# Performance work log

Hardware: AMD Instinct MI355X
Metric: run time of the kernel (lower is better)

The kernel has to match this reference:

```python
import jax, jax.numpy as jnp
import numpy as np

B, T, I, H, O, F = 256, 2048, 64, 256, 64, 16
NUM_LAYERS = 2


def setup_inputs() -> dict:
    key = jax.random.key(0)
    ks = jax.random.split(key, 12)
    s = 1.0 / np.sqrt(H)  # PyTorch RNN/Linear init scale
    u = lambda k, shp: jax.random.uniform(k, shp, jnp.float32, -s, s)
    return {
        "x": jax.random.normal(ks[0], (B, T, I), jnp.float32),
        "hidden": jnp.zeros((NUM_LAYERS, B, H), jnp.float32),
        "W_ih0": u(ks[1], (H, I)),
        "W_hh0": u(ks[2], (H, H)),
        "b_ih0": u(ks[3], (H,)),
        "b_hh0": u(ks[4], (H,)),
        "W_ih1": u(ks[5], (H, H)),
        "W_hh1": u(ks[6], (H, H)),
        "b_ih1": u(ks[7], (H,)),
        "b_hh1": u(ks[8], (H,)),
        "fc_W": u(ks[9], (O, H)),
        "fc_b": u(ks[10], (O,)),
        "future_timesegments": F,
    }


def _rnn_layer(xs, h0, W_ih, W_hh, b_ih, b_hh):
    # xs: [T, B, in_dim]; h0: [B, H]
    # Precompute input contribution for all timesteps (one big GEMM),
    # then scan only the sequential recurrence h@W_hh^T + tanh.
    pre = jnp.einsum('tbi,hi->tbh', xs, W_ih) + b_ih + b_hh  # [T, B, H]

    def step(h, p_t):
        h_new = jnp.tanh(p_t + h @ W_hh.T)
        return h_new, h_new

    h_T, ys = jax.lax.scan(step, h0, pre)
    return ys, h_T  # ys: [T, B, H]


def reference(x, hidden, W_ih0, W_hh0, b_ih0, b_hh0,
              W_ih1, W_hh1, b_ih1, b_hh1, fc_W, fc_b,
              future_timesegments):
    xs = jnp.swapaxes(x, 0, 1)  # [T, B, I] (batch_first -> time major)
    ys0, h0 = _rnn_layer(xs, hidden[0], W_ih0, W_hh0, b_ih0, b_hh0)
    ys1, h1 = _rnn_layer(ys0, hidden[1], W_ih1, W_hh1, b_ih1, b_hh1)
    # out[:, -F:, :] in batch-first layout
    tail = jnp.swapaxes(ys1[-future_timesegments:], 0, 1)  # [B, F, H]
    out = tail @ fc_W.T + fc_b  # [B, F, O]
    new_hidden = jnp.stack([h0, h1])  # [num_layers, B, H]
    return out, new_hidden
```

## Files before the change

### kernel.cpp

```cpp
#include <hip/hip_runtime.h>

#define BB 256
#define TT 2048
#define II 64
#define HH 256
#define OO 64
#define FF 16


#define BUFSZ 2048
#define BUF0 0
#define BUF1 BUFSZ
#define H1OFF 704
#define XOFF 1344
#define SLICE 80
#define TAILOFF (2 * BUFSZ)
#define LDSBYTES (TAILOFF + FF * HH * 2)

typedef _Float16 h2 __attribute__((ext_vector_type(2)));
typedef _Float16 h8 __attribute__((ext_vector_type(8)));

__device__ __forceinline__ float fdot2f(h2 a, h2 b, float c) {
#if __has_builtin(__builtin_amdgcn_fdot2)
  return __builtin_amdgcn_fdot2(a, b, c, false);
#else
  return c + (float)a[0] * (float)b[0] + (float)a[1] * (float)b[1];
#endif
}

__device__ __forceinline__ float fast_tanh(float z) {
  float e = __builtin_amdgcn_exp2f(z * 2.885390081777927f);
  return 1.0f - 2.0f * __builtin_amdgcn_rcpf(e + 1.0f);
}

__device__ __forceinline__ h2 i2h(int w) {
  union { int i; h2 h; } u; u.i = w; return u.h;
}
__device__ __forceinline__ int pk2i(const float* p) {
  union { h2 h; int i; } u; u.h[0] = (_Float16)p[0]; u.h[1] = (_Float16)p[1];
  return u.i;
}

template <int CTRL>
__device__ __forceinline__ float dpp_add(float v) {
  union { float f; int i; } a, r;
  a.f = v;
  r.i = __builtin_amdgcn_update_dpp(0, a.i, CTRL, 0xF, 0xF, true);
  return v + r.f;
}
__device__ __forceinline__ float swz4_add(float v) {
  union { float f; int i; } a, r;
  a.f = v;
  r.i = __builtin_amdgcn_ds_swizzle(a.i, 0x101F);
  return v + r.f;
}

#define RNN_STEP(T, RB, WB)                                                    \
  {                                                                            \
    float xn = 0.f;                                                            \
    if (kg == 0) {                                                             \
      int tn = (T) + 1 < TT ? (T) + 1 : (T);                                   \
      xn = xrow[(size_t)tn * II + xi];                                         \
    }                                                                          \
    float a0[4] = {0.f, 0.f, 0.f, 0.f};                                        \
    float a1[4] = {0.f, 0.f, 0.f, 0.f};                                        \
    {                                                                          \
      const int4 xv = *(const int4*)(xaddr + (RB) + XOFF);                     \
      _Pragma("unroll") for (int r = 0; r < 4; ++r) {                          \
        a0[r] = fdot2f(i2h(xv.x), i2h(w0x[r][0]), a0[r]);                      \
        a0[r] = fdot2f(i2h(xv.y), i2h(w0x[r][1]), a0[r]);                      \
        a0[r] = fdot2f(i2h(xv.z), i2h(w0x[r][2]), a0[r]);                      \
        a0[r] = fdot2f(i2h(xv.w), i2h(w0x[r][3]), a0[r]);                      \
      }                                                                        \
    }                                                                          \
    _Pragma("unroll") for (int c = 0; c < 4; ++c) {                            \
      const int4 v = *(const int4*)(haddr + (RB) + c * 16);                    \
      _Pragma("unroll") for (int r = 0; r < 4; ++r) {                          \
        a0[r] = fdot2f(i2h(v.x), i2h(w0h[r][4 * c + 0]), a0[r]);               \
        a0[r] = fdot2f(i2h(v.y), i2h(w0h[r][4 * c + 1]), a0[r]);               \
        a0[r] = fdot2f(i2h(v.z), i2h(w0h[r][4 * c + 2]), a0[r]);               \
        a0[r] = fdot2f(i2h(v.w), i2h(w0h[r][4 * c + 3]), a0[r]);               \
        a1[r] = fdot2f(i2h(v.x), i2h(w1g[r][4 * c + 0]), a1[r]);               \
        a1[r] = fdot2f(i2h(v.y), i2h(w1g[r][4 * c + 1]), a1[r]);               \
        a1[r] = fdot2f(i2h(v.z), i2h(w1g[r][4 * c + 2]), a1[r]);               \
        a1[r] = fdot2f(i2h(v.w), i2h(w1g[r][4 * c + 3]), a1[r]);               \
      }                                                                        \
    }                                                                          \
    _Pragma("unroll") for (int c = 0; c < 4; ++c) {                            \
      const int4 v = *(const int4*)(haddr + (RB) + H1OFF + c * 16);            \
      _Pragma("unroll") for (int r = 0; r < 4; ++r) {                          \
        a1[r] = fdot2f(i2h(v.x), i2h(w1h[r][4 * c + 0]), a1[r]);               \
        a1[r] = fdot2f(i2h(v.y), i2h(w1h[r][4 * c + 1]), a1[r]);               \
        a1[r] = fdot2f(i2h(v.z), i2h(w1h[r][4 * c + 2]), a1[r]);               \
        a1[r] = fdot2f(i2h(v.w), i2h(w1h[r][4 * c + 3]), a1[r]);               \
      }                                                                        \
    }                                                                          \
    _Pragma("unroll") for (int r = 0; r < 4; ++r) {                            \
      a0[r] = dpp_add<0xB1>(a0[r]);                                            \
      a0[r] = dpp_add<0x4E>(a0[r]);                                            \
      a0[r] = swz4_add(a0[r]);                                                 \
      a1[r] = dpp_add<0xB1>(a1[r]);                                            \
      a1[r] = dpp_add<0x4E>(a1[r]);                                            \
      a1[r] = swz4_add(a1[r]);                                                 \
    }                                                                          \
    float s0 = (kg & 1) ? a0[1] : a0[0];                                       \
    float s1 = (kg & 1) ? a0[3] : a0[2];                                       \
    float u0 = (kg & 1) ? a1[1] : a1[0];                                       \
    float u1 = (kg & 1) ? a1[3] : a1[2];                                       \
    float v0 = (kg & 2) ? s1 : s0;                                             \
    float v1 = (kg & 2) ? u1 : u0;                                             \
    float hnew = fast_tanh((L ? v1 : v0) + mybias);                            \
    hlast = hnew;                                                              \
    if ((T) > 0 || L == 0) *(_Float16*)(waddr + (WB)) = (_Float16)hnew;        \
    if (L == 1 && (T) >= TT - FF + 1)                                          \
      *(_Float16*)(tailaddr + ((T) - (TT - FF + 1)) * (HH * 2)) =              \
          (_Float16)hnew;                                                      \
    if (kg == 0) *(_Float16*)(lb + (WB) + XOFF + xi * 2) = (_Float16)xn;       \
    __syncthreads();                                                           \
  }

__global__ __attribute__((amdgpu_flat_work_group_size(512, 512),
                          amdgpu_waves_per_eu(2, 2)))
void rnn_fused(const float* __restrict__ x, const float* __restrict__ hidden,
               const float* __restrict__ Wih0, const float* __restrict__ Whh0,
               const float* __restrict__ bih0, const float* __restrict__ bhh0,
               const float* __restrict__ Wih1, const float* __restrict__ Whh1,
               const float* __restrict__ bih1, const float* __restrict__ bhh1,
               const float* __restrict__ fcW, const float* __restrict__ fcb,
               float* __restrict__ out)
{
  const int tid = threadIdx.x;
  const int b = blockIdx.x;
  const int lane = tid & 63;
  const int kg = lane & 7;
  const int rg = (tid >> 6) * 8 + (lane >> 3);
  const int j0 = rg * 4;
  const int L = kg >> 2;
  const int cj = j0 + (kg & 3);
  const int xi = tid >> 3;

  __shared__ __align__(16) char lds[LDSBYTES];
  char* lb = (char*)lds;

  int w0x[4][4], w0h[4][16], w1g[4][16], w1h[4][16];
#pragma unroll
  for (int r = 0; r < 4; ++r) {
    const float* p0 = Wih0 + (size_t)(j0 + r) * II + kg * 8;
#pragma unroll
    for (int m = 0; m < 4; ++m) w0x[r][m] = pk2i(p0 + 2 * m);
    const float* p1 = Whh0 + (size_t)(j0 + r) * HH + kg * 32;
#pragma unroll
    for (int m = 0; m < 16; ++m) w0h[r][m] = pk2i(p1 + 2 * m);
    const float* p2 = Wih1 + (size_t)(j0 + r) * HH + kg * 32;
#pragma unroll
    for (int m = 0; m < 16; ++m) w1g[r][m] = pk2i(p2 + 2 * m);
    const float* p3 = Whh1 + (size_t)(j0 + r) * HH + kg * 32;
#pragma unroll
    for (int m = 0; m < 16; ++m) w1h[r][m] = pk2i(p3 + 2 * m);
  }
#pragma unroll
  for (int r = 0; r < 4; ++r) {
#pragma unroll
    for (int m = 0; m < 4; ++m) asm volatile("" : "+v"(w0x[r][m]));
#pragma unroll
    for (int m = 0; m < 16; ++m) {
      asm volatile("" : "+v"(w0h[r][m]));
      asm volatile("" : "+v"(w1g[r][m]));
      asm volatile("" : "+v"(w1h[r][m]));
    }
  }
  float mybias = L ? (bih1[cj] + bhh1[cj]) : (bih0[cj] + bhh0[cj]);
  asm volatile("" : "+v"(mybias));

  const char* haddr = lb + kg * SLICE;
  const char* xaddr = lb + kg * 16;
  char* waddr = lb + L * H1OFF + (cj >> 5) * SLICE + (cj & 31) * 2;
  char* tailaddr = lb + TAILOFF + cj * 2;

  if (tid < HH) {
    char* p = lb + (tid >> 5) * SLICE + (tid & 31) * 2;
    _Float16 h0v = (_Float16)hidden[(size_t)b * HH + tid];
    _Float16 h1v = (_Float16)hidden[(size_t)(BB + b) * HH + tid];
    *(_Float16*)(p + BUF0) = h0v;
    *(_Float16*)(p + BUF0 + H1OFF) = h1v;
    *(_Float16*)(p + BUF1 + H1OFF) = h1v;
  }
  const float* xrow = x + (size_t)b * TT * II;
  if (tid < II) *(_Float16*)(lb + BUF0 + XOFF + tid * 2) = (_Float16)xrow[tid];
  float hlast = 0.f, h1last = 0.f;
  __syncthreads();

#pragma unroll 1
  for (int t = 0; t < TT; t += 2) {
    RNN_STEP(t, BUF0, BUF1)
    RNN_STEP(t + 1, BUF1, BUF0)
  }

  {
    float a1[4] = {0.f, 0.f, 0.f, 0.f};
#pragma unroll
    for (int c = 0; c < 4; ++c) {
      const int4 v = *(const int4*)(haddr + BUF0 + c * 16);
#pragma unroll
      for (int r = 0; r < 4; ++r) {
        a1[r] = fdot2f(i2h(v.x), i2h(w1g[r][4 * c + 0]), a1[r]);
        a1[r] = fdot2f(i2h(v.y), i2h(w1g[r][4 * c + 1]), a1[r]);
        a1[r] = fdot2f(i2h(v.z), i2h(w1g[r][4 * c + 2]), a1[r]);
        a1[r] = fdot2f(i2h(v.w), i2h(w1g[r][4 * c + 3]), a1[r]);
      }
    }
#pragma unroll
    for (int c = 0; c < 4; ++c) {
      const int4 v = *(const int4*)(haddr + BUF0 + H1OFF + c * 16);
#pragma unroll
      for (int r = 0; r < 4; ++r) {
        a1[r] = fdot2f(i2h(v.x), i2h(w1h[r][4 * c + 0]), a1[r]);
        a1[r] = fdot2f(i2h(v.y), i2h(w1h[r][4 * c + 1]), a1[r]);
        a1[r] = fdot2f(i2h(v.z), i2h(w1h[r][4 * c + 2]), a1[r]);
        a1[r] = fdot2f(i2h(v.w), i2h(w1h[r][4 * c + 3]), a1[r]);
      }
    }
#pragma unroll
    for (int r = 0; r < 4; ++r) {
      a1[r] = dpp_add<0xB1>(a1[r]);
      a1[r] = dpp_add<0x4E>(a1[r]);
      a1[r] = swz4_add(a1[r]);
    }
    float u0 = (kg & 1) ? a1[1] : a1[0];
    float u1 = (kg & 1) ? a1[3] : a1[2];
    float v1 = (kg & 2) ? u1 : u0;
    float h1e = fast_tanh(v1 + mybias);
    h1last = h1e;
    if (L == 1) *(_Float16*)(tailaddr + (FF - 1) * (HH * 2)) = (_Float16)h1e;
  }
  __syncthreads();

  if (L == 0) out[BB * FF * OO + (size_t)b * HH + cj] = hlast;
  else        out[BB * FF * OO + (size_t)(BB + b) * HH + cj] = h1last;

  const int o = tid & 63;
  const int fg = tid >> 6;
  const _Float16* tp = (const _Float16*)(lb + TAILOFF);
  float acc0 = 0.f, acc1 = 0.f;
  const float* wrow = fcW + o * HH;
  for (int c = 0; c < HH / 8; ++c) {
    float wv[8];
#pragma unroll
    for (int k = 0; k < 8; ++k) wv[k] = wrow[8 * c + k];
    h8 q0 = *(const h8*)(tp + (2 * fg) * HH + 8 * c);
    h8 q1 = *(const h8*)(tp + (2 * fg + 1) * HH + 8 * c);
#pragma unroll
    for (int e = 0; e < 8; ++e) {
      acc0 += (float)q0[e] * wv[e];
      acc1 += (float)q1[e] * wv[e];
    }
  }
  const float bo = fcb[o];
  out[((size_t)b * FF + 2 * fg) * OO + o] = acc0 + bo;
  out[((size_t)b * FF + 2 * fg + 1) * OO + o] = acc1 + bo;
}

extern "C" void kernel_launch(void* const* d_in, const int* in_sizes, int n_in,
                              void* d_out, int out_size, void* d_ws, size_t ws_size,
                              hipStream_t stream) {
  (void)in_sizes; (void)n_in; (void)d_ws; (void)ws_size; (void)out_size;
  rnn_fused<<<dim3(BB), dim3(512), 0, stream>>>(
      (const float*)d_in[0],  (const float*)d_in[1],
      (const float*)d_in[2],  (const float*)d_in[3],
      (const float*)d_in[4],  (const float*)d_in[5],
      (const float*)d_in[6],  (const float*)d_in[7],
      (const float*)d_in[8],  (const float*)d_in[9],
      (const float*)d_in[10], (const float*)d_in[11],
      (float*)d_out);
}
```

Baseline: 3.280 ms.

## Repartition RNN step to 4-way K split with 2 rows per thread

Changes the per-thread work split from an 8-way reduction split over 4 output rows to a 4-way split over 2 rows per thread, with longer K slices (64 elements). This removes the ds_swizzle reduction stage, leaving only two DPP adds, and cuts the select logic. The LDS layout of the hidden state and x is restrided to match. Dot products now go through inline-asm v_dot2_f32_f16. Weight registers per thread stay about the same, but each thread's serial dot-product chain doubles in length, which may lengthen the critical path of each sequential step.

```diff
diff --git a/kernel.cpp b/kernel.cpp
--- a/kernel.cpp
+++ b/kernel.cpp
@@ -8,24 +8,20 @@
 #define FF 16
 
 
-#define BUFSZ 2048
+#define BUFSZ 1280
 #define BUF0 0
 #define BUF1 BUFSZ
-#define H1OFF 704
-#define XOFF 1344
-#define SLICE 80
+#define H1OFF 576
+#define XOFF 1152
+#define HSL 144
+#define XSL 32
 #define TAILOFF (2 * BUFSZ)
 #define LDSBYTES (TAILOFF + FF * HH * 2)
 
-typedef _Float16 h2 __attribute__((ext_vector_type(2)));
 typedef _Float16 h8 __attribute__((ext_vector_type(8)));
 
-__device__ __forceinline__ float fdot2f(h2 a, h2 b, float c) {
-#if __has_builtin(__builtin_amdgcn_fdot2)
-  return __builtin_amdgcn_fdot2(a, b, c, false);
-#else
-  return c + (float)a[0] * (float)b[0] + (float)a[1] * (float)b[1];
-#endif
+__device__ __forceinline__ void adot(float& acc, int hv, int wv) {
+  asm("v_dot2_f32_f16 %0, %1, %2, %0" : "+v"(acc) : "v"(hv), "v"(wv));
 }
 
 __device__ __forceinline__ float fast_tanh(float z) {
@@ -33,11 +29,9 @@
   return 1.0f - 2.0f * __builtin_amdgcn_rcpf(e + 1.0f);
 }
 
-__device__ __forceinline__ h2 i2h(int w) {
-  union { int i; h2 h; } u; u.i = w; return u.h;
-}
 __device__ __forceinline__ int pk2i(const float* p) {
-  union { h2 h; int i; } u; u.h[0] = (_Float16)p[0]; u.h[1] = (_Float16)p[1];
+  union { _Float16 h[2]; int i; } u;
+  u.h[0] = (_Float16)p[0]; u.h[1] = (_Float16)p[1];
   return u.i;
 }
 
@@ -48,74 +42,55 @@
   r.i = __builtin_amdgcn_update_dpp(0, a.i, CTRL, 0xF, 0xF, true);
   return v + r.f;
 }
-__device__ __forceinline__ float swz4_add(float v) {
-  union { float f; int i; } a, r;
-  a.f = v;
-  r.i = __builtin_amdgcn_ds_swizzle(a.i, 0x101F);
-  return v + r.f;
-}
 
 #define RNN_STEP(T, RB, WB)                                                    \
   {                                                                            \
     float xn = 0.f;                                                            \
-    if (kg == 0) {                                                             \
+    if ((tid & 7) == 0) {                                                      \
       int tn = (T) + 1 < TT ? (T) + 1 : (T);                                   \
       xn = xrow[(size_t)tn * II + xi];                                         \
     }                                                                          \
-    float a0[4] = {0.f, 0.f, 0.f, 0.f};                                        \
-    float a1[4] = {0.f, 0.f, 0.f, 0.f};                                        \
-    {                                                                          \
-      const int4 xv = *(const int4*)(xaddr + (RB) + XOFF);                     \
-      _Pragma("unroll") for (int r = 0; r < 4; ++r) {                          \
-        a0[r] = fdot2f(i2h(xv.x), i2h(w0x[r][0]), a0[r]);                      \
-        a0[r] = fdot2f(i2h(xv.y), i2h(w0x[r][1]), a0[r]);                      \
-        a0[r] = fdot2f(i2h(xv.z), i2h(w0x[r][2]), a0[r]);                      \
-        a0[r] = fdot2f(i2h(xv.w), i2h(w0x[r][3]), a0[r]);                      \
-      }                                                                        \
-    }                                                                          \
-    _Pragma("unroll") for (int c = 0; c < 4; ++c) {                            \
-      const int4 v = *(const int4*)(haddr + (RB) + c * 16);                    \
-      _Pragma("unroll") for (int r = 0; r < 4; ++r) {                          \
-        a0[r] = fdot2f(i2h(v.x), i2h(w0h[r][4 * c + 0]), a0[r]);               \
-        a0[r] = fdot2f(i2h(v.y), i2h(w0h[r][4 * c + 1]), a0[r]);               \
-        a0[r] = fdot2f(i2h(v.z), i2h(w0h[r][4 * c + 2]), a0[r]);               \
-        a0[r] = fdot2f(i2h(v.w), i2h(w0h[r][4 * c + 3]), a0[r]);               \
-        a1[r] = fdot2f(i2h(v.x), i2h(w1g[r][4 * c + 0]), a1[r]);               \
-        a1[r] = fdot2f(i2h(v.y), i2h(w1g[r][4 * c + 1]), a1[r]);               \
-        a1[r] = fdot2f(i2h(v.z), i2h(w1g[r][4 * c + 2]), a1[r]);               \
-        a1[r] = fdot2f(i2h(v.w), i2h(w1g[r][4 * c + 3]), a1[r]);               \
-      }                                                                        \
-    }                                                                          \
-    _Pragma("unroll") for (int c = 0; c < 4; ++c) {                            \
-      const int4 v = *(const int4*)(haddr + (RB) + H1OFF + c * 16);            \
-      _Pragma("unroll") for (int r = 0; r < 4; ++r) {                          \
-        a1[r] = fdot2f(i2h(v.x), i2h(w1h[r][4 * c + 0]), a1[r]);               \
-        a1[r] = fdot2f(i2h(v.y), i2h(w1h[r][4 * c + 1]), a1[r]);               \
-        a1[r] = fdot2f(i2h(v.z), i2h(w1h[r][4 * c + 2]), a1[r]);               \
-        a1[r] = fdot2f(i2h(v.w), i2h(w1h[r][4 * c + 3]), a1[r]);               \
-      }                                                                        \
-    }                                                                          \
-    _Pragma("unroll") for (int r = 0; r < 4; ++r) {                            \
-      a0[r] = dpp_add<0xB1>(a0[r]);                                            \
-      a0[r] = dpp_add<0x4E>(a0[r]);                                            \
-      a0[r] = swz4_add(a0[r]);                                                 \
-      a1[r] = dpp_add<0xB1>(a1[r]);                                            \
-      a1[r] = dpp_add<0x4E>(a1[r]);                                            \
-      a1[r] = swz4_add(a1[r]);                                                 \
-    }                                                                          \
-    float s0 = (kg & 1) ? a0[1] : a0[0];                                       \
-    float s1 = (kg & 1) ? a0[3] : a0[2];                                       \
-    float u0 = (kg & 1) ? a1[1] : a1[0];                                       \
-    float u1 = (kg & 1) ? a1[3] : a1[2];                                       \
-    float v0 = (kg & 2) ? s1 : s0;                                             \
-    float v1 = (kg & 2) ? u1 : u0;                                             \
+    float a00 = 0.f, a01 = 0.f, a10 = 0.f, a11 = 0.f;                          \
+    _Pragma("unroll") for (int c = 0; c < 2; ++c) {                            \
+      const int4 v = *(const int4*)(xaddr + (RB) + c * 16);                    \
+      adot(a00, v.x, w0x[0][4 * c + 0]); adot(a00, v.y, w0x[0][4 * c + 1]);    \
+      adot(a00, v.z, w0x[0][4 * c + 2]); adot(a00, v.w, w0x[0][4 * c + 3]);    \
+      adot(a01, v.x, w0x[1][4 * c + 0]); adot(a01, v.y, w0x[1][4 * c + 1]);    \
+      adot(a01, v.z, w0x[1][4 * c + 2]); adot(a01, v.w, w0x[1][4 * c + 3]);    \
+    }                                                                          \
+    _Pragma("unroll") for (int c = 0; c < 8; ++c) {                            \
+      const int4 v = *(const int4*)(h0addr + (RB) + c * 16);                   \
+      adot(a00, v.x, w0h[0][4 * c + 0]); adot(a00, v.y, w0h[0][4 * c + 1]);    \
+      adot(a00, v.z, w0h[0][4 * c + 2]); adot(a00, v.w, w0h[0][4 * c + 3]);    \
+      adot(a01, v.x, w0h[1][4 * c + 0]); adot(a01, v.y, w0h[1][4 * c + 1]);    \
+      adot(a01, v.z, w0h[1][4 * c + 2]); adot(a01, v.w, w0h[1][4 * c + 3]);    \
+      adot(a10, v.x, w1g[0][4 * c + 0]); adot(a10, v.y, w1g[0][4 * c + 1]);    \
+      adot(a10, v.z, w1g[0][4 * c + 2]); adot(a10, v.w, w1g[0][4 * c + 3]);    \
+      adot(a11, v.x, w1g[1][4 * c + 0]); adot(a11, v.y, w1g[1][4 * c + 1]);    \
+      adot(a11, v.z, w1g[1][4 * c + 2]); adot(a11, v.w, w1g[1][4 * c + 3]);    \
+    }                                                                          \
+    _Pragma("unroll") for (int c = 0; c < 8; ++c) {                            \
+      const int4 v = *(const int4*)(h0addr + (RB) + H1OFF + c * 16);           \
+      adot(a10, v.x, w1h[0][4 * c + 0]); adot(a10, v.y, w1h[0][4 * c + 1]);    \
+      adot(a10, v.z, w1h[0][4 * c + 2]); adot(a10, v.w, w1h[0][4 * c + 3]);    \
+      adot(a11, v.x, w1h[1][4 * c + 0]); adot(a11, v.y, w1h[1][4 * c + 1]);    \
+      adot(a11, v.z, w1h[1][4 * c + 2]); adot(a11, v.w, w1h[1][4 * c + 3]);    \
+    }                                                                          \
+    a00 = dpp_add<0xB1>(a00); a00 = dpp_add<0x4E>(a00);                        \
+    a01 = dpp_add<0xB1>(a01); a01 = dpp_add<0x4E>(a01);                        \
+    a10 = dpp_add<0xB1>(a10); a10 = dpp_add<0x4E>(a10);                        \
+    a11 = dpp_add<0xB1>(a11); a11 = dpp_add<0x4E>(a11);                        \
+    float v0 = (kg & 1) ? a01 : a00;                                           \
+    float v1 = (kg & 1) ? a11 : a10;                                           \
     float hnew = fast_tanh((L ? v1 : v0) + mybias);                            \
     hlast = hnew;                                                              \
     if ((T) > 0 || L == 0) *(_Float16*)(waddr + (WB)) = (_Float16)hnew;        \
     if (L == 1 && (T) >= TT - FF + 1)                                          \
       *(_Float16*)(tailaddr + ((T) - (TT - FF + 1)) * (HH * 2)) =              \
           (_Float16)hnew;                                                      \
-    if (kg == 0) *(_Float16*)(lb + (WB) + XOFF + xi * 2) = (_Float16)xn;       \
+    if ((tid & 7) == 0)                                                        \
+      *(_Float16*)(lb + (WB) + XOFF + (xi >> 4) * XSL + (xi & 15) * 2) =       \
+          (_Float16)xn;                                                        \
     __syncthreads();                                                           \
   }
 
@@ -132,38 +107,38 @@
   const int tid = threadIdx.x;
   const int b = blockIdx.x;
   const int lane = tid & 63;
-  const int kg = lane & 7;
-  const int rg = (tid >> 6) * 8 + (lane >> 3);
-  const int j0 = rg * 4;
-  const int L = kg >> 2;
-  const int cj = j0 + (kg & 3);
+  const int kg = lane & 3;
+  const int rg = tid >> 2;
+  const int j0 = rg * 2;
+  const int L = kg >> 1;
+  const int cj = j0 + (kg & 1);
   const int xi = tid >> 3;
 
   __shared__ __align__(16) char lds[LDSBYTES];
   char* lb = (char*)lds;
 
-  int w0x[4][4], w0h[4][16], w1g[4][16], w1h[4][16];
-#pragma unroll
-  for (int r = 0; r < 4; ++r) {
-    const float* p0 = Wih0 + (size_t)(j0 + r) * II + kg * 8;
-#pragma unroll
-    for (int m = 0; m < 4; ++m) w0x[r][m] = pk2i(p0 + 2 * m);
-    const float* p1 = Whh0 + (size_t)(j0 + r) * HH + kg * 32;
-#pragma unroll
-    for (int m = 0; m < 16; ++m) w0h[r][m] = pk2i(p1 + 2 * m);
-    const float* p2 = Wih1 + (size_t)(j0 + r) * HH + kg * 32;
-#pragma unroll
-    for (int m = 0; m < 16; ++m) w1g[r][m] = pk2i(p2 + 2 * m);
-    const float* p3 = Whh1 + (size_t)(j0 + r) * HH + kg * 32;
-#pragma unroll
-    for (int m = 0; m < 16; ++m) w1h[r][m] = pk2i(p3 + 2 * m);
-  }
-#pragma unroll
-  for (int r = 0; r < 4; ++r) {
-#pragma unroll
-    for (int m = 0; m < 4; ++m) asm volatile("" : "+v"(w0x[r][m]));
-#pragma unroll
-    for (int m = 0; m < 16; ++m) {
+  int w0x[2][8], w0h[2][32], w1g[2][32], w1h[2][32];
+#pragma unroll
+  for (int r = 0; r < 2; ++r) {
+    const float* p0 = Wih0 + (size_t)(j0 + r) * II + kg * 16;
+#pragma unroll
+    for (int m = 0; m < 8; ++m) w0x[r][m] = pk2i(p0 + 2 * m);
+    const float* p1 = Whh0 + (size_t)(j0 + r) * HH + kg * 64;
+#pragma unroll
+    for (int m = 0; m < 32; ++m) w0h[r][m] = pk2i(p1 + 2 * m);
+    const float* p2 = Wih1 + (size_t)(j0 + r) * HH + kg * 64;
+#pragma unroll
+    for (int m = 0; m < 32; ++m) w1g[r][m] = pk2i(p2 + 2 * m);
+    const float* p3 = Whh1 + (size_t)(j0 + r) * HH + kg * 64;
+#pragma unroll
+    for (int m = 0; m < 32; ++m) w1h[r][m] = pk2i(p3 + 2 * m);
+  }
+#pragma unroll
+  for (int r = 0; r < 2; ++r) {
+#pragma unroll
+    for (int m = 0; m < 8; ++m) asm volatile("" : "+v"(w0x[r][m]));
+#pragma unroll
+    for (int m = 0; m < 32; ++m) {
       asm volatile("" : "+v"(w0h[r][m]));
       asm volatile("" : "+v"(w1g[r][m]));
       asm volatile("" : "+v"(w1h[r][m]));
@@ -172,13 +147,13 @@
   float mybias = L ? (bih1[cj] + bhh1[cj]) : (bih0[cj] + bhh0[cj]);
   asm volatile("" : "+v"(mybias));
 
-  const char* haddr = lb + kg * SLICE;
-  const char* xaddr = lb + kg * 16;
-  char* waddr = lb + L * H1OFF + (cj >> 5) * SLICE + (cj & 31) * 2;
+  const char* h0addr = lb + kg * HSL;
+  const char* xaddr = lb + XOFF + kg * XSL;
+  char* waddr = lb + (L ? H1OFF : 0) + (cj >> 6) * HSL + (cj & 63) * 2;
   char* tailaddr = lb + TAILOFF + cj * 2;
 
   if (tid < HH) {
-    char* p = lb + (tid >> 5) * SLICE + (tid & 31) * 2;
+    char* p = lb + (tid >> 6) * HSL + (tid & 63) * 2;
     _Float16 h0v = (_Float16)hidden[(size_t)b * HH + tid];
     _Float16 h1v = (_Float16)hidden[(size_t)(BB + b) * HH + tid];
     *(_Float16*)(p + BUF0) = h0v;
@@ -186,7 +161,9 @@
     *(_Float16*)(p + BUF1 + H1OFF) = h1v;
   }
   const float* xrow = x + (size_t)b * TT * II;
-  if (tid < II) *(_Float16*)(lb + BUF0 + XOFF + tid * 2) = (_Float16)xrow[tid];
+  if (tid < II)
+    *(_Float16*)(lb + BUF0 + XOFF + (tid >> 4) * XSL + (tid & 15) * 2) =
+        (_Float16)xrow[tid];
   float hlast = 0.f, h1last = 0.f;
   __syncthreads();
 
@@ -197,38 +174,26 @@
   }
 
   {
-    float a1[4] = {0.f, 0.f, 0.f, 0.f};
-#pragma unroll
-    for (int c = 0; c < 4; ++c) {
-      const int4 v = *(const int4*)(haddr + BUF0 + c * 16);
-#pragma unroll
-      for (int r = 0; r < 4; ++r) {
-        a1[r] = fdot2f(i2h(v.x), i2h(w1g[r][4 * c + 0]), a1[r]);
-        a1[r] = fdot2f(i2h(v.y), i2h(w1g[r][4 * c + 1]), a1[r]);
-        a1[r] = fdot2f(i2h(v.z), i2h(w1g[r][4 * c + 2]), a1[r]);
-        a1[r] = fdot2f(i2h(v.w), i2h(w1g[r][4 * c + 3]), a1[r]);
-      }
-    }
-#pragma unroll
-    for (int c = 0; c < 4; ++c) {
-      const int4 v = *(const int4*)(haddr + BUF0 + H1OFF + c * 16);
-#pragma unroll
-      for (int r = 0; r < 4; ++r) {
-        a1[r] = fdot2f(i2h(v.x), i2h(w1h[r][4 * c + 0]), a1[r]);
-        a1[r] = fdot2f(i2h(v.y), i2h(w1h[r][4 * c + 1]), a1[r]);
-        a1[r] = fdot2f(i2h(v.z), i2h(w1h[r][4 * c + 2]), a1[r]);
-        a1[r] = fdot2f(i2h(v.w), i2h(w1h[r][4 * c + 3]), a1[r]);
-      }
-    }
-#pragma unroll
-    for (int r = 0; r < 4; ++r) {
-      a1[r] = dpp_add<0xB1>(a1[r]);
-      a1[r] = dpp_add<0x4E>(a1[r]);
-      a1[r] = swz4_add(a1[r]);
-    }
-    float u0 = (kg & 1) ? a1[1] : a1[0];
-    float u1 = (kg & 1) ? a1[3] : a1[2];
-    float v1 = (kg & 2) ? u1 : u0;
+    float a10 = 0.f, a11 = 0.f;
+#pragma unroll
+    for (int c = 0; c < 8; ++c) {
+      const int4 v = *(const int4*)(h0addr + BUF0 + c * 16);
+      adot(a10, v.x, w1g[0][4 * c + 0]); adot(a10, v.y, w1g[0][4 * c + 1]);
+      adot(a10, v.z, w1g[0][4 * c + 2]); adot(a10, v.w, w1g[0][4 * c + 3]);
+      adot(a11, v.x, w1g[1][4 * c + 0]); adot(a11, v.y, w1g[1][4 * c + 1]);
+      adot(a11, v.z, w1g[1][4 * c + 2]); adot(a11, v.w, w1g[1][4 * c + 3]);
+    }
+#pragma unroll
+    for (int c = 0; c < 8; ++c) {
+      const int4 v = *(const int4*)(h0addr + BUF0 + H1OFF + c * 16);
+      adot(a10, v.x, w1h[0][4 * c + 0]); adot(a10, v.y, w1h[0][4 * c + 1]);
+      adot(a10, v.z, w1h[0][4 * c + 2]); adot(a10, v.w, w1h[0][4 * c + 3]);
+      adot(a11, v.x, w1h[1][4 * c + 0]); adot(a11, v.y, w1h[1][4 * c + 1]);
+      adot(a11, v.z, w1h[1][4 * c + 2]); adot(a11, v.w, w1h[1][4 * c + 3]);
+    }
+    a10 = dpp_add<0xB1>(a10); a10 = dpp_add<0x4E>(a10);
+    a11 = dpp_add<0xB1>(a11); a11 = dpp_add<0x4E>(a11);
+    float v1 = (kg & 1) ? a11 : a10;
     float h1e = fast_tanh(v1 + mybias);
     h1last = h1e;
     if (L == 1) *(_Float16*)(tailaddr + (FF - 1) * (HH * 2)) = (_Float16)h1e;
```

New measurement: 3.146 ms. -4.1%, faster.

## Split fused two-layer RNN into per-layer kernels with chunked workspace streaming

Applied to the files above, without the earlier changes.

Replaces the single kernel, which advanced both layers in lockstep (half the lanes on layer 0, half on layer 1), with two kernels. `rnn_l0` runs the layer-0 recurrence and streams fp16 hidden states to the workspace. `rnn_l1` then consumes those states for the layer-1 recurrence and computes the FC head. Each kernel now gives all eight K-groups to a single layer, which shortens the per-step dot products. Time is chunked to fit the workspace, and layer-1 state is carried between chunks. The cost is that the two recurrences no longer overlap, so the number of sequential steps doubles, and global-memory traffic for the streamed hidden states is added.

```diff
diff --git a/kernel.cpp b/kernel.cpp
--- a/kernel.cpp
+++ b/kernel.cpp
@@ -8,39 +8,23 @@
 #define FF 16
 
 
-#define BUFSZ 2048
-#define BUF0 0
-#define BUF1 BUFSZ
-#define H1OFF 704
-#define XOFF 1344
-#define SLICE 80
-#define TAILOFF (2 * BUFSZ)
-#define LDSBYTES (TAILOFF + FF * HH * 2)
-
 typedef _Float16 h2 __attribute__((ext_vector_type(2)));
 typedef _Float16 h8 __attribute__((ext_vector_type(8)));
 
 __device__ __forceinline__ float fdot2f(h2 a, h2 b, float c) {
-#if __has_builtin(__builtin_amdgcn_fdot2)
   return __builtin_amdgcn_fdot2(a, b, c, false);
-#else
-  return c + (float)a[0] * (float)b[0] + (float)a[1] * (float)b[1];
-#endif
-}
-
+}
+__device__ __forceinline__ h2 i2h(int w) {
+  union { int i; h2 h; } u; u.i = w; return u.h;
+}
+__device__ __forceinline__ int pk2i(const float* p) {
+  union { h2 h; int i; } u; u.h[0] = (_Float16)p[0]; u.h[1] = (_Float16)p[1];
+  return u.i;
+}
 __device__ __forceinline__ float fast_tanh(float z) {
   float e = __builtin_amdgcn_exp2f(z * 2.885390081777927f);
   return 1.0f - 2.0f * __builtin_amdgcn_rcpf(e + 1.0f);
 }
-
-__device__ __forceinline__ h2 i2h(int w) {
-  union { int i; h2 h; } u; u.i = w; return u.h;
-}
-__device__ __forceinline__ int pk2i(const float* p) {
-  union { h2 h; int i; } u; u.h[0] = (_Float16)p[0]; u.h[1] = (_Float16)p[1];
-  return u.i;
-}
-
 template <int CTRL>
 __device__ __forceinline__ float dpp_add(float v) {
   union { float f; int i; } a, r;
@@ -48,199 +32,238 @@
   r.i = __builtin_amdgcn_update_dpp(0, a.i, CTRL, 0xF, 0xF, true);
   return v + r.f;
 }
-__device__ __forceinline__ float swz4_add(float v) {
-  union { float f; int i; } a, r;
-  a.f = v;
-  r.i = __builtin_amdgcn_ds_swizzle(a.i, 0x101F);
-  return v + r.f;
-}
-
-#define RNN_STEP(T, RB, WB)                                                    \
+
+#define P1_HB(i) ((i) * 640)
+#define P1_XB(i) (1280 + (i) * 128)
+
+#define L0_STEP(T, RB, WB)                                                     \
   {                                                                            \
     float xn = 0.f;                                                            \
-    if (kg == 0) {                                                             \
-      int tn = (T) + 1 < TT ? (T) + 1 : (T);                                   \
-      xn = xrow[(size_t)tn * II + xi];                                         \
-    }                                                                          \
-    float a0[4] = {0.f, 0.f, 0.f, 0.f};                                        \
-    float a1[4] = {0.f, 0.f, 0.f, 0.f};                                        \
+    if ((tid & 7) == 0) {                                                      \
+      int tg = tstart + (T) + 1; if (tg > TT - 1) tg = TT - 1;                 \
+      xn = xrow[(size_t)tg * II + xi];                                         \
+    }                                                                          \
+    float aa[4] = {0.f, 0.f, 0.f, 0.f};                                        \
     {                                                                          \
-      const int4 xv = *(const int4*)(xaddr + (RB) + XOFF);                     \
+      const int4 xv = *(const int4*)(lb + P1_XB(RB) + kg * 16);                \
       _Pragma("unroll") for (int r = 0; r < 4; ++r) {                          \
-        a0[r] = fdot2f(i2h(xv.x), i2h(w0x[r][0]), a0[r]);                      \
-        a0[r] = fdot2f(i2h(xv.y), i2h(w0x[r][1]), a0[r]);                      \
-        a0[r] = fdot2f(i2h(xv.z), i2h(w0x[r][2]), a0[r]);                      \
-        a0[r] = fdot2f(i2h(xv.w), i2h(w0x[r][3]), a0[r]);                      \
+        aa[r] = fdot2f(i2h(xv.x), i2h(w0x[r][0]), aa[r]);                      \
+        aa[r] = fdot2f(i2h(xv.y), i2h(w0x[r][1]), aa[r]);                      \
+        aa[r] = fdot2f(i2h(xv.z), i2h(w0x[r][2]), aa[r]);                      \
+        aa[r] = fdot2f(i2h(xv.w), i2h(w0x[r][3]), aa[r]);                      \
       }                                                                        \
     }                                                                          \
     _Pragma("unroll") for (int c = 0; c < 4; ++c) {                            \
-      const int4 v = *(const int4*)(haddr + (RB) + c * 16);                    \
+      const int4 v = *(const int4*)(lb + P1_HB(RB) + kg * 80 + c * 16);        \
       _Pragma("unroll") for (int r = 0; r < 4; ++r) {                          \
-        a0[r] = fdot2f(i2h(v.x), i2h(w0h[r][4 * c + 0]), a0[r]);               \
-        a0[r] = fdot2f(i2h(v.y), i2h(w0h[r][4 * c + 1]), a0[r]);               \
-        a0[r] = fdot2f(i2h(v.z), i2h(w0h[r][4 * c + 2]), a0[r]);               \
-        a0[r] = fdot2f(i2h(v.w), i2h(w0h[r][4 * c + 3]), a0[r]);               \
-        a1[r] = fdot2f(i2h(v.x), i2h(w1g[r][4 * c + 0]), a1[r]);               \
-        a1[r] = fdot2f(i2h(v.y), i2h(w1g[r][4 * c + 1]), a1[r]);               \
-        a1[r] = fdot2f(i2h(v.z), i2h(w1g[r][4 * c + 2]), a1[r]);               \
-        a1[r] = fdot2f(i2h(v.w), i2h(w1g[r][4 * c + 3]), a1[r]);               \
+        aa[r] = fdot2f(i2h(v.x), i2h(w0h[r][4 * c + 0]), aa[r]);               \
+        aa[r] = fdot2f(i2h(v.y), i2h(w0h[r][4 * c + 1]), aa[r]);               \
+        aa[r] = fdot2f(i2h(v.z), i2h(w0h[r][4 * c + 2]), aa[r]);               \
+        aa[r] = fdot2f(i2h(v.w), i2h(w0h[r][4 * c + 3]), aa[r]);               \
       }                                                                        \
     }                                                                          \
-    _Pragma("unroll") for (int c = 0; c < 4; ++c) {                            \
-      const int4 v = *(const int4*)(haddr + (RB) + H1OFF + c * 16);            \
-      _Pragma("unroll") for (int r = 0; r < 4; ++r) {                          \
-        a1[r] = fdot2f(i2h(v.x), i2h(w1h[r][4 * c + 0]), a1[r]);               \
-        a1[r] = fdot2f(i2h(v.y), i2h(w1h[r][4 * c + 1]), a1[r]);               \
-        a1[r] = fdot2f(i2h(v.z), i2h(w1h[r][4 * c + 2]), a1[r]);               \
-        a1[r] = fdot2f(i2h(v.w), i2h(w1h[r][4 * c + 3]), a1[r]);               \
-      }                                                                        \
-    }                                                                          \
     _Pragma("unroll") for (int r = 0; r < 4; ++r) {                            \
-      a0[r] = dpp_add<0xB1>(a0[r]);                                            \
-      a0[r] = dpp_add<0x4E>(a0[r]);                                            \
-      a0[r] = swz4_add(a0[r]);                                                 \
-      a1[r] = dpp_add<0xB1>(a1[r]);                                            \
-      a1[r] = dpp_add<0x4E>(a1[r]);                                            \
-      a1[r] = swz4_add(a1[r]);                                                 \
-    }                                                                          \
-    float s0 = (kg & 1) ? a0[1] : a0[0];                                       \
-    float s1 = (kg & 1) ? a0[3] : a0[2];                                       \
-    float u0 = (kg & 1) ? a1[1] : a1[0];                                       \
-    float u1 = (kg & 1) ? a1[3] : a1[2];                                       \
-    float v0 = (kg & 2) ? s1 : s0;                                             \
-    float v1 = (kg & 2) ? u1 : u0;                                             \
-    float hnew = fast_tanh((L ? v1 : v0) + mybias);                            \
-    hlast = hnew;                                                              \
-    if ((T) > 0 || L == 0) *(_Float16*)(waddr + (WB)) = (_Float16)hnew;        \
-    if (L == 1 && (T) >= TT - FF + 1)                                          \
-      *(_Float16*)(tailaddr + ((T) - (TT - FF + 1)) * (HH * 2)) =              \
+      aa[r] = dpp_add<0xB1>(aa[r]); aa[r] = dpp_add<0x4E>(aa[r]);              \
+      aa[r] = dpp_add<0x141>(aa[r]);                                           \
+    }                                                                          \
+    float s0 = (kg & 1) ? aa[1] : aa[0];                                       \
+    float s1 = (kg & 1) ? aa[3] : aa[2];                                       \
+    float hnew = fast_tanh(((kg & 2) ? s1 : s0) + mybias);                     \
+    if (kg < 4) {                                                              \
+      *(_Float16*)(lb + P1_HB(WB) + (cj >> 5) * 80 + (cj & 31) * 2) =          \
           (_Float16)hnew;                                                      \
-    if (kg == 0) *(_Float16*)(lb + (WB) + XOFF + xi * 2) = (_Float16)xn;       \
+      hstream[(bt + (T)) * HH + cj] = (_Float16)hnew;                          \
+      if (tstart + (T) == TT - 1) h0keep = hnew;                               \
+    }                                                                          \
+    if ((tid & 7) == 0)                                                        \
+      *(_Float16*)(lb + P1_XB(WB) + (xi >> 3) * 16 + (xi & 7) * 2) =           \
+          (_Float16)xn;                                                        \
     __syncthreads();                                                           \
   }
 
 __global__ __attribute__((amdgpu_flat_work_group_size(512, 512),
                           amdgpu_waves_per_eu(2, 2)))
-void rnn_fused(const float* __restrict__ x, const float* __restrict__ hidden,
-               const float* __restrict__ Wih0, const float* __restrict__ Whh0,
-               const float* __restrict__ bih0, const float* __restrict__ bhh0,
-               const float* __restrict__ Wih1, const float* __restrict__ Whh1,
-               const float* __restrict__ bih1, const float* __restrict__ bhh1,
-               const float* __restrict__ fcW, const float* __restrict__ fcb,
-               float* __restrict__ out)
+void rnn_l0(const float* __restrict__ x, const float* __restrict__ hidden,
+            const float* __restrict__ Wih0, const float* __restrict__ Whh0,
+            const float* __restrict__ bih0, const float* __restrict__ bhh0,
+            _Float16* __restrict__ hstream, float* __restrict__ out,
+            int tstart, int tcount)
 {
   const int tid = threadIdx.x;
   const int b = blockIdx.x;
-  const int lane = tid & 63;
-  const int kg = lane & 7;
-  const int rg = (tid >> 6) * 8 + (lane >> 3);
-  const int j0 = rg * 4;
-  const int L = kg >> 2;
-  const int cj = j0 + (kg & 3);
+  const int kg = tid & 7;
+  const int r0 = (tid >> 3) * 4;
+  const int cj = r0 + (kg & 3);
   const int xi = tid >> 3;
 
-  __shared__ __align__(16) char lds[LDSBYTES];
+  __shared__ __align__(16) char lds[1536];
   char* lb = (char*)lds;
-
-  int w0x[4][4], w0h[4][16], w1g[4][16], w1h[4][16];
+  const size_t bt = (size_t)b * tcount;
+
+  int w0x[4][4], w0h[4][16];
 #pragma unroll
   for (int r = 0; r < 4; ++r) {
-    const float* p0 = Wih0 + (size_t)(j0 + r) * II + kg * 8;
+    const float* p0 = Wih0 + (size_t)(r0 + r) * II + kg * 8;
 #pragma unroll
     for (int m = 0; m < 4; ++m) w0x[r][m] = pk2i(p0 + 2 * m);
-    const float* p1 = Whh0 + (size_t)(j0 + r) * HH + kg * 32;
+    const float* p1 = Whh0 + (size_t)(r0 + r) * HH + kg * 32;
 #pragma unroll
     for (int m = 0; m < 16; ++m) w0h[r][m] = pk2i(p1 + 2 * m);
-    const float* p2 = Wih1 + (size_t)(j0 + r) * HH + kg * 32;
+  }
+#pragma unroll
+  for (int r = 0; r < 4; ++r) {
+#pragma unroll
+    for (int m = 0; m < 4; ++m) asm volatile("" : "+v"(w0x[r][m]));
+#pragma unroll
+    for (int m = 0; m < 16; ++m) asm volatile("" : "+v"(w0h[r][m]));
+  }
+  float mybias = bih0[cj] + bhh0[cj];
+  asm volatile("" : "+v"(mybias));
+
+  const float* xrow = x + (size_t)b * TT * II;
+
+  if (tid < HH) {
+    _Float16 hv = (tstart == 0)
+        ? (_Float16)hidden[(size_t)b * HH + tid]
+        : hstream[(bt + (tcount - 1)) * HH + tid];
+    *(_Float16*)(lb + P1_HB(0) + (tid >> 5) * 80 + (tid & 31) * 2) = hv;
+  }
+  if (tid < II)
+    *(_Float16*)(lb + P1_XB(0) + (tid >> 3) * 16 + (tid & 7) * 2) =
+        (_Float16)xrow[(size_t)tstart * II + tid];
+  float h0keep = 0.f;
+  __syncthreads();
+
+#pragma unroll 1
+  for (int t = 0; t < tcount; t += 2) {
+    L0_STEP(t, 0, 1)
+    L0_STEP(t + 1, 1, 0)
+  }
+
+  if (tstart + tcount == TT && kg < 4)
+    out[BB * FF * OO + (size_t)b * HH + cj] = h0keep;
+}
+
+#define P2_GB(i) ((i) * 640)
+#define P2_HB(i) (1280 + (i) * 640)
+#define P2_TAIL 2560
+
+#define L1_STEP(T, RB, WB)                                                     \
+  {                                                                            \
+    int gn = 0;                                                                \
+    if (tid < 128) {                                                           \
+      int tn = (T) + 1; if (tn > tcount - 1) tn = tcount - 1;                  \
+      gn = gi[(bt + tn) * 128 + tid];                                          \
+    }                                                                          \
+    float aa[4] = {0.f, 0.f, 0.f, 0.f};                                        \
+    _Pragma("unroll") for (int c = 0; c < 4; ++c) {                            \
+      const int4 v = *(const int4*)(lb + P2_GB(RB) + kg * 80 + c * 16);        \
+      _Pragma("unroll") for (int r = 0; r < 4; ++r) {                          \
+        aa[r] = fdot2f(i2h(v.x), i2h(w1g[r][4 * c + 0]), aa[r]);               \
+        aa[r] = fdot2f(i2h(v.y), i2h(w1g[r][4 * c + 1]), aa[r]);               \
+        aa[r] = fdot2f(i2h(v.z), i2h(w1g[r][4 * c + 2]), aa[r]);               \
+        aa[r] = fdot2f(i2h(v.w), i2h(w1g[r][4 * c + 3]), aa[r]);               \
+      }                                                                        \
+    }                                                                          \
+    _Pragma("unroll") for (int c = 0; c < 4; ++c) {                            \
+      const int4 v = *(const int4*)(lb + P2_HB(RB) + kg * 80 + c * 16);        \
+      _Pragma("unroll") for (int r = 0; r < 4; ++r) {                          \
+        aa[r] = fdot2f(i2h(v.x), i2h(w1h[r][4 * c + 0]), aa[r]);               \
+        aa[r] = fdot2f(i2h(v.y), i2h(w1h[r][4 * c + 1]), aa[r]);               \
+        aa[r] = fdot2f(i2h(v.z), i2h(w1h[r][4 * c + 2]), aa[r]);               \
+        aa[r] = fdot2f(i2h(v.w), i2h(w1h[r][4 * c + 3]), aa[r]);               \
+      }                                                                        \
+    }                                                                          \
+    _Pragma("unroll") for (int r = 0; r < 4; ++r) {                            \
+      aa[r] = dpp_add<0xB1>(aa[r]); aa[r] = dpp_add<0x4E>(aa[r]);              \
+      aa[r] = dpp_add<0x141>(aa[r]);                                           \
+    }                                                                          \
+    float s0 = (kg & 1) ? aa[1] : aa[0];                                       \
+    float s1 = (kg & 1) ? aa[3] : aa[2];                                       \
+    float hnew = fast_tanh(((kg & 2) ? s1 : s0) + mybias);                     \
+    if (kg < 4) {                                                              \
+      *(_Float16*)(lb + P2_HB(WB) + (cj >> 5) * 80 + (cj & 31) * 2) =          \
+          (_Float16)hnew;                                                      \
+      if (lastchunk && (T) >= tcount - FF)                                     \
+        *(_Float16*)(lb + P2_TAIL + ((T) - (tcount - FF)) * 512 + cj * 2) =    \
+            (_Float16)hnew;                                                    \
+      if (lastchunk && (T) == tcount - 1) h1keep = hnew;                       \
+    }                                                                          \
+    if (tid < 128)                                                             \
+      *(int*)(lb + P2_GB(WB) + (tid >> 4) * 80 + (tid & 15) * 4) = gn;         \
+    __syncthreads();                                                           \
+  }
+
+__global__ __attribute__((amdgpu_flat_work_group_size(512, 512),
+                          amdgpu_waves_per_eu(2, 2)))
+void rnn_l1(const float* __restrict__ hidden, const float* __restrict__ Wih1,
+            const float* __restrict__ Whh1, const float* __restrict__ bih1,
+            const float* __restrict__ bhh1, const float* __restrict__ fcW,
+            const float* __restrict__ fcb, const _Float16* __restrict__ hstream,
+            _Float16* __restrict__ h1carry, float* __restrict__ out,
+            int tstart, int tcount)
+{
+  const int tid = threadIdx.x;
+  const int b = blockIdx.x;
+  const int kg = tid & 7;
+  const int r0 = (tid >> 3) * 4;
+  const int cj = r0 + (kg & 3);
+  const bool lastchunk = (tstart + tcount == TT);
+
+  __shared__ __align__(16) char lds[10752];
+  char* lb = (char*)lds;
+  const size_t bt = (size_t)b * tcount;
+  const int* gi = (const int*)hstream;
+
+  int w1g[4][16], w1h[4][16];
+#pragma unroll
+  for (int r = 0; r < 4; ++r) {
+    const float* p2 = Wih1 + (size_t)(r0 + r) * HH + kg * 32;
 #pragma unroll
     for (int m = 0; m < 16; ++m) w1g[r][m] = pk2i(p2 + 2 * m);
-    const float* p3 = Whh1 + (size_t)(j0 + r) * HH + kg * 32;
+    const float* p3 = Whh1 + (size_t)(r0 + r) * HH + kg * 32;
 #pragma unroll
     for (int m = 0; m < 16; ++m) w1h[r][m] = pk2i(p3 + 2 * m);
   }
 #pragma unroll
   for (int r = 0; r < 4; ++r) {
 #pragma unroll
-    for (int m = 0; m < 4; ++m) asm volatile("" : "+v"(w0x[r][m]));
-#pragma unroll
     for (int m = 0; m < 16; ++m) {
-      asm volatile("" : "+v"(w0h[r][m]));
       asm volatile("" : "+v"(w1g[r][m]));
       asm volatile("" : "+v"(w1h[r][m]));
     }
   }
-  float mybias = L ? (bih1[cj] + bhh1[cj]) : (bih0[cj] + bhh0[cj]);
+  float mybias = bih1[cj] + bhh1[cj];
   asm volatile("" : "+v"(mybias));
 
-  const char* haddr = lb + kg * SLICE;
-  const char* xaddr = lb + kg * 16;
-  char* waddr = lb + L * H1OFF + (cj >> 5) * SLICE + (cj & 31) * 2;
-  char* tailaddr = lb + TAILOFF + cj * 2;
-
   if (tid < HH) {
-    char* p = lb + (tid >> 5) * SLICE + (tid & 31) * 2;
-    _Float16 h0v = (_Float16)hidden[(size_t)b * HH + tid];
-    _Float16 h1v = (_Float16)hidden[(size_t)(BB + b) * HH + tid];
-    *(_Float16*)(p + BUF0) = h0v;
-    *(_Float16*)(p + BUF0 + H1OFF) = h1v;
-    *(_Float16*)(p + BUF1 + H1OFF) = h1v;
-  }
-  const float* xrow = x + (size_t)b * TT * II;
-  if (tid < II) *(_Float16*)(lb + BUF0 + XOFF + tid * 2) = (_Float16)xrow[tid];
-  float hlast = 0.f, h1last = 0.f;
+    _Float16 hv = (tstart == 0)
+        ? (_Float16)hidden[(size_t)(BB + b) * HH + tid]
+        : h1carry[(size_t)b * HH + tid];
+    *(_Float16*)(lb + P2_HB(0) + (tid >> 5) * 80 + (tid & 31) * 2) = hv;
+  }
+  if (tid < 128)
+    *(int*)(lb + P2_GB(0) + (tid >> 4) * 80 + (tid & 15) * 4) = gi[bt * 128 + tid];
+  float h1keep = 0.f;
   __syncthreads();
 
 #pragma unroll 1
-  for (int t = 0; t < TT; t += 2) {
-    RNN_STEP(t, BUF0, BUF1)
-    RNN_STEP(t + 1, BUF1, BUF0)
-  }
-
-  {
-    float a1[4] = {0.f, 0.f, 0.f, 0.f};
-#pragma unroll
-    for (int c = 0; c < 4; ++c) {
-      const int4 v = *(const int4*)(haddr + BUF0 + c * 16);
-#pragma unroll
-      for (int r = 0; r < 4; ++r) {
-        a1[r] = fdot2f(i2h(v.x), i2h(w1g[r][4 * c + 0]), a1[r]);
-        a1[r] = fdot2f(i2h(v.y), i2h(w1g[r][4 * c + 1]), a1[r]);
-        a1[r] = fdot2f(i2h(v.z), i2h(w1g[r][4 * c + 2]), a1[r]);
-        a1[r] = fdot2f(i2h(v.w), i2h(w1g[r][4 * c + 3]), a1[r]);
-      }
-    }
-#pragma unroll
-    for (int c = 0; c < 4; ++c) {
-      const int4 v = *(const int4*)(haddr + BUF0 + H1OFF + c * 16);
-#pragma unroll
-      for (int r = 0; r < 4; ++r) {
-        a1[r] = fdot2f(i2h(v.x), i2h(w1h[r][4 * c + 0]), a1[r]);
-        a1[r] = fdot2f(i2h(v.y), i2h(w1h[r][4 * c + 1]), a1[r]);
-        a1[r] = fdot2f(i2h(v.z), i2h(w1h[r][4 * c + 2]), a1[r]);
-        a1[r] = fdot2f(i2h(v.w), i2h(w1h[r][4 * c + 3]), a1[r]);
-      }
-    }
-#pragma unroll
-    for (int r = 0; r < 4; ++r) {
-      a1[r] = dpp_add<0xB1>(a1[r]);
-      a1[r] = dpp_add<0x4E>(a1[r]);
-      a1[r] = swz4_add(a1[r]);
-    }
-    float u0 = (kg & 1) ? a1[1] : a1[0];
-    float u1 = (kg & 1) ? a1[3] : a1[2];
-    float v1 = (kg & 2) ? u1 : u0;
-    float h1e = fast_tanh(v1 + mybias);
-    h1last = h1e;
-    if (L == 1) *(_Float16*)(tailaddr + (FF - 1) * (HH * 2)) = (_Float16)h1e;
-  }
-  __syncthreads();
-
-  if (L == 0) out[BB * FF * OO + (size_t)b * HH + cj] = hlast;
-  else        out[BB * FF * OO + (size_t)(BB + b) * HH + cj] = h1last;
+  for (int t = 0; t < tcount; t += 2) {
+    L1_STEP(t, 0, 1)
+    L1_STEP(t + 1, 1, 0)
+  }
+
+  if (tid < HH)
+    h1carry[(size_t)b * HH + tid] =
+        *(_Float16*)(lb + P2_HB(0) + (tid >> 5) * 80 + (tid & 31) * 2);
+
+  if (!lastchunk) return;
+
+  if (kg < 4) out[BB * FF * OO + (size_t)(BB + b) * HH + cj] = h1keep;
 
   const int o = tid & 63;
   const int fg = tid >> 6;
-  const _Float16* tp = (const _Float16*)(lb + TAILOFF);
+  const _Float16* tp = (const _Float16*)(lb + P2_TAIL);
   float acc0 = 0.f, acc1 = 0.f;
   const float* wrow = fcW + o * HH;
   for (int c = 0; c < HH / 8; ++c) {
@@ -263,13 +286,33 @@
 extern "C" void kernel_launch(void* const* d_in, const int* in_sizes, int n_in,
                               void* d_out, int out_size, void* d_ws, size_t ws_size,
                               hipStream_t stream) {
-  (void)in_sizes; (void)n_in; (void)d_ws; (void)ws_size; (void)out_size;
-  rnn_fused<<<dim3(BB), dim3(512), 0, stream>>>(
-      (const float*)d_in[0],  (const float*)d_in[1],
-      (const float*)d_in[2],  (const float*)d_in[3],
-      (const float*)d_in[4],  (const float*)d_in[5],
-      (const float*)d_in[6],  (const float*)d_in[7],
-      (const float*)d_in[8],  (const float*)d_in[9],
-      (const float*)d_in[10], (const float*)d_in[11],
-      (float*)d_out);
-}
+  (void)in_sizes; (void)n_in; (void)out_size;
+  const float* x    = (const float*)d_in[0];
+  const float* hid  = (const float*)d_in[1];
+  const float* Wih0 = (const float*)d_in[2];
+  const float* Whh0 = (const float*)d_in[3];
+  const float* bih0 = (const float*)d_in[4];
+  const float* bhh0 = (const float*)d_in[5];
+  const float* Wih1 = (const float*)d_in[6];
+  const float* Whh1 = (const float*)d_in[7];
+  const float* bih1 = (const float*)d_in[8];
+  const float* bhh1 = (const float*)d_in[9];
+  const float* fcW  = (const float*)d_in[10];
+  const float* fcb  = (const float*)d_in[11];
+  float* out = (float*)d_out;
+
+  size_t tch = 2048;
+  while (tch > 2 &&
+         ((size_t)BB * tch * HH * 2 + (size_t)BB * HH * 2) > ws_size)
+    tch >>= 1;
+  _Float16* hstream = (_Float16*)d_ws;
+  _Float16* h1carry = (_Float16*)d_ws + (size_t)BB * tch * HH;
+
+  for (int ts = 0; ts < TT; ts += (int)tch) {
+    rnn_l0<<<dim3(BB), dim3(512), 0, stream>>>(
+        x, hid, Wih0, Whh0, bih0, bhh0, hstream, out, ts, (int)tch);
+    rnn_l1<<<dim3(BB), dim3(512), 0, stream>>>(
+        hid, Wih1, Whh1, bih1, bhh1, fcW, fcb, hstream, h1carry, out,
+        ts, (int)tch);
+  }
+}
```

New measurement: 3.605 ms. 1.1x slower.
